# Kernel tuning notes

Hardware: AMD Instinct MI355X
Metric: run time of the kernel (lower is better)

Reference implementation:

```python
import jax, jax.numpy as jnp
import numpy as np

N_EMBD = 1024
N_HEAD = 16
HEAD_DIM = N_EMBD // N_HEAD


def setup_inputs() -> dict:
    key = jax.random.key(0)
    k1, k2, k3, k4, k5 = jax.random.split(key, 5)
    x = jax.random.normal(k1, (4, 2048, N_EMBD), dtype=jnp.float32)
    s = 1.0 / np.sqrt(N_EMBD)
    W_attn = jax.random.normal(k2, (N_EMBD, 3 * N_EMBD), dtype=jnp.float32) * s
    b_attn = jnp.zeros((3 * N_EMBD,), dtype=jnp.float32)
    W_proj = jax.random.normal(k3, (N_EMBD, N_EMBD), dtype=jnp.float32) * s
    b_proj = jnp.zeros((N_EMBD,), dtype=jnp.float32)
    return {"x": x, "W_attn": W_attn, "b_attn": b_attn, "W_proj": W_proj, "b_proj": b_proj}


def _attention(x, W_attn, b_attn, W_proj, b_proj):
    B, T, C = x.shape
    qkv = jnp.einsum("btc,cd->btd", x, W_attn) + b_attn  # [B,T,3C]
    q, k, v = jnp.split(qkv, 3, axis=-1)
    # [B,T,C] -> [B,H,T,D]
    def heads(t):
        return t.reshape(B, T, N_HEAD, HEAD_DIM).transpose(0, 2, 1, 3)
    q, k, v = heads(q), heads(k), heads(v)
    scale = 1.0 / np.sqrt(HEAD_DIM)
    scores = jnp.einsum("bhqd,bhkd->bhqk", q, k) * scale  # [B,H,T,T]
    causal = jnp.tril(jnp.ones((T, T), dtype=bool))
    scores = jnp.where(causal, scores, jnp.finfo(scores.dtype).min)
    attn = jax.nn.softmax(scores, axis=-1)
    y = jnp.einsum("bhqk,bhkd->bhqd", attn, v)  # [B,H,T,D]
    y = y.transpose(0, 2, 1, 3).reshape(B, T, C)
    return jnp.einsum("btc,cd->btd", y, W_proj) + b_proj


def reference(x, W_attn, b_attn, W_proj, b_proj):
    return _attention(x, W_attn, b_attn, W_proj, b_proj)
```

## Files before the change

### kernel.cpp

```cpp
#include <hip/hip_runtime.h>
#include <hip/hip_bf16.h>

#define BB 4
#define TT 2048
#define CC 1024
#define HH 16
#define DD 64
#define BT (BB*TT)
#define C3 (3*CC)
#define LDST 72
#define QSCALE 0.18033688011112042f

typedef __attribute__((ext_vector_type(8))) short short8;
typedef __attribute__((ext_vector_type(4))) float f32x4;

__device__ __forceinline__ short f2bs(float f) {
  __hip_bfloat16 h = __float2bfloat16(f);
  return *reinterpret_cast<short*>(&h);
}

__device__ __forceinline__ void gl_lds16(const short* g, short* l) {
  __builtin_amdgcn_global_load_lds(
      (const __attribute__((address_space(1))) void*)(g),
      (__attribute__((address_space(3))) void*)(l), 16, 0, 0);
}

__global__ __launch_bounds__(256)
void prep(const float* __restrict__ Wa, short* __restrict__ Wat,
          const float* __restrict__ Wp, short* __restrict__ Wpt,
          const float* __restrict__ x, short* __restrict__ Xb)
{
  __shared__ float Lt[64][65];
  const int bx = blockIdx.x;
  if (bx >= 64) {
    size_t chunk = (size_t)(bx - 64) * 16 + blockIdx.y;
    size_t i = (chunk * 256 + threadIdx.x) * 8;
    float4 a = *reinterpret_cast<const float4*>(x + i);
    float4 b = *reinterpret_cast<const float4*>(x + i + 4);
    short8 o;
    o[0] = f2bs(a.x); o[1] = f2bs(a.y); o[2] = f2bs(a.z); o[3] = f2bs(a.w);
    o[4] = f2bs(b.x); o[5] = f2bs(b.y); o[6] = f2bs(b.z); o[7] = f2bs(b.w);
    *reinterpret_cast<short8*>(Xb + i) = o;
    return;
  }
  const bool isA = (bx < 48);
  const float* in  = isA ? Wa  : Wp;
  short*       out = isA ? Wat : Wpt;
  const int N  = isA ? C3 : CC;
  const int n0 = (isA ? bx : bx - 48) * 64;
  const int k0 = blockIdx.y * 64;
  const int cx = threadIdx.x & 15, rr = threadIdx.x >> 4;
#pragma unroll
  for (int p = 0; p < 4; ++p) {
    int kr = p * 16 + rr;
    float4 u = *reinterpret_cast<const float4*>(in + (size_t)(k0 + kr) * N + n0 + cx * 4);
    Lt[kr][cx * 4 + 0] = u.x;
    Lt[kr][cx * 4 + 1] = u.y;
    Lt[kr][cx * 4 + 2] = u.z;
    Lt[kr][cx * 4 + 3] = u.w;
  }
  __syncthreads();
#pragma unroll
  for (int p = 0; p < 4; ++p) {
    int nr = p * 16 + rr;
    short4 o;
    o.x = f2bs(Lt[cx * 4 + 0][nr]);
    o.y = f2bs(Lt[cx * 4 + 1][nr]);
    o.z = f2bs(Lt[cx * 4 + 2][nr]);
    o.w = f2bs(Lt[cx * 4 + 3][nr]);
    *reinterpret_cast<short4*>(out + (size_t)(n0 + nr) * CC + k0 + cx * 4) = o;
  }
}

template<bool QKV>
__global__ __launch_bounds__(512, 2)
void gemm256(const short* __restrict__ A, const short* __restrict__ Bt,
             const float* __restrict__ bias,
             short* __restrict__ qb, short* __restrict__ kb, short* __restrict__ vb,
             float* __restrict__ out)
{
  __shared__ __align__(16) short SMEM[65536];

  const int t = threadIdx.x;
  const int lane = t & 63;
  const int l16 = lane & 15, quad = lane >> 4;
  const int w = t >> 6;
  const int wr = w >> 2, wc = w & 3;

  const int per   = gridDim.x >> 3;
  const int chunk = (blockIdx.x & 7) * per + (blockIdx.x >> 3);
  const int NBC   = QKV ? 12 : 4;
  const int brow  = chunk / NBC, bcol = chunk % NBC;
  const int row0  = brow * 256;
  const int col0  = bcol * 256;

  auto stageQ = [&](int bufS, int kcS, int tileS, bool isA) __attribute__((always_inline)) {
#pragma unroll
    for (int l = 0; l < 2; ++l) {
      int gq = l * 512 + t;
      int rq = gq >> 2;
      int g  = (gq & 3) ^ ((rq >> 1) & 3);
      if (isA) {
        gl_lds16(A + (size_t)(row0 + rq) * CC + tileS * 64 + kcS * 32 + g * 8,
                 &SMEM[bufS * 16384 + kcS * 8192 + gq * 8]);
      } else {
        gl_lds16(Bt + (size_t)(col0 + rq) * CC + tileS * 64 + kcS * 32 + g * 8,
                 &SMEM[32768 + bufS * 16384 + kcS * 8192 + gq * 8]);
      }
    }
  };

  f32x4 acc[8][4];
#pragma unroll
  for (int i = 0; i < 8; ++i)
#pragma unroll
    for (int j = 0; j < 4; ++j) acc[i][j] = (f32x4){0.f, 0.f, 0.f, 0.f};

  auto kTile = [&](int u, int cb, int tm) __attribute__((always_inline)) {
    const short* Ac = &SMEM[cb * 16384];
    const short* Bc = &SMEM[32768 + cb * 16384];
    short8 bf[4];
#pragma unroll
    for (int ph = 0; ph < 4; ++ph) {
      const int kc = ph >> 1, q = ph & 1;
      if (q == 0) {
#pragma unroll
        for (int j = 0; j < 4; ++j) {
          int rb = wc * 64 + j * 16 + l16;
          bf[j] = *reinterpret_cast<const short8*>(
              &Bc[kc * 8192 + rb * 32 + (((quad ^ (rb >> 1)) & 3) << 3)]);
        }
      }
      short8 af[4];
#pragma unroll
      for (int iq = 0; iq < 4; ++iq) {
        int ra = wr * 128 + (q * 4 + iq) * 16 + l16;
        af[iq] = *reinterpret_cast<const short8*>(
            &Ac[kc * 8192 + ra * 32 + (((quad ^ (ra >> 1)) & 3) << 3)]);
      }

      if      (ph == 0) { if (tm < 2) stageQ(cb ^ 1, 1, u + 1, true ); }
      else if (ph == 1) { if (tm < 2) stageQ(cb ^ 1, 1, u + 1, false); }
      else if (ph == 2) { if (tm < 1) stageQ(cb,     0, u + 2, true ); }
      else              { if (tm < 1) stageQ(cb,     0, u + 2, false); }

      __builtin_amdgcn_s_barrier();
      asm volatile("s_waitcnt lgkmcnt(0)" ::: "memory");
      __builtin_amdgcn_sched_barrier(0);

      __builtin_amdgcn_s_setprio(1);
#pragma unroll
      for (int iq = 0; iq < 4; ++iq)
#pragma unroll
        for (int j = 0; j < 4; ++j)
          acc[q * 4 + iq][j] =
              __builtin_amdgcn_mfma_f32_16x16x32_bf16(af[iq], bf[j], acc[q * 4 + iq][j], 0, 0, 0);
      __builtin_amdgcn_s_setprio(0);

      if (ph == 1) {
        if (tm == 2) { asm volatile("s_waitcnt vmcnt(0)" ::: "memory"); }
        else         { asm volatile("s_waitcnt vmcnt(8)" ::: "memory"); }
      } else if (ph == 3) {
        if      (tm == 0) { asm volatile("s_waitcnt vmcnt(8)" ::: "memory"); }
        else if (tm == 1) { asm volatile("s_waitcnt vmcnt(4)" ::: "memory"); }
      }
      __builtin_amdgcn_s_barrier();
    }
  };

  stageQ(0, 0, 0, true);  stageQ(0, 0, 0, false);
  stageQ(0, 1, 0, true);  stageQ(0, 1, 0, false);
  stageQ(1, 0, 1, true);  stageQ(1, 0, 1, false);
  asm volatile("s_waitcnt vmcnt(8)" ::: "memory");
  __builtin_amdgcn_s_barrier();

  for (int u = 0; u < 14; u += 2) {
    kTile(u,     0, 0);
    kTile(u + 1, 1, 0);
  }
  kTile(14, 0, 1);
  kTile(15, 1, 2);

  if constexpr (QKV) {
    const int sel = col0 >> 10;
#pragma unroll
    for (int hp = 0; hp < 2; ++hp) {
      __syncthreads();
      if (wr == hp) {
#pragma unroll
        for (int j = 0; j < 4; ++j) {
          const int colL = wc * 64 + j * 16 + l16;
          const float bv = bias[col0 + colL];
#pragma unroll
          for (int i = 0; i < 8; ++i)
#pragma unroll
            for (int r = 0; r < 4; ++r) {
              const int rl = i * 16 + quad * 4 + r;
              float val = acc[i][j][r] + bv;
              if (sel == 0) val *= QSCALE;
              short vs = f2bs(val);
              if (sel == 2) {
                int tpl = (rl & ~63) | ((rl & 15) << 2) | ((rl >> 4) & 3);
                SMEM[colL * 136 + tpl] = vs;
              } else {
                SMEM[rl * 264 + colL] = vs;
              }
            }
        }
      }
      __syncthreads();
      const int Rbase = row0 + hp * 128;
      const int bi = Rbase >> 11;
      if (sel != 2) {
        short* __restrict__ dstB = (sel == 0) ? qb : kb;
#pragma unroll
        for (int rep = 0; rep < 8; ++rep) {
          int slot = rep * 512 + t;
          int rl = slot >> 5, ch = slot & 31;
          short8 vv = *reinterpret_cast<const short8*>(&SMEM[rl * 264 + ch * 8]);
          int tt  = (Rbase & 2047) + rl;
          int cin = (col0 + ch * 8) & 1023;
          int h = cin >> 6, dd = cin & 63;
          *reinterpret_cast<short8*>(
              &dstB[(((size_t)(bi * HH + h)) * TT + tt) * DD + dd]) = vv;
        }
      } else {
#pragma unroll
        for (int rep = 0; rep < 8; ++rep) {
          int slot = rep * 512 + t;
          int dcol = slot >> 4, ch = slot & 15;
          short8 vv = *reinterpret_cast<const short8*>(&SMEM[dcol * 136 + ch * 8]);
          int cin = (col0 + dcol) & 1023;
          int h = cin >> 6, dd = cin & 63;
          int ttb = (Rbase & 2047) + ch * 8;
          *reinterpret_cast<short8*>(
              &vb[(((size_t)(bi * HH + h)) * DD + dd) * TT + ttb]) = vv;
        }
      }
    }
  } else {
#pragma unroll
    for (int j = 0; j < 4; ++j) {
      int col = col0 + wc * 64 + j * 16 + l16;
      float bv = bias[col];
#pragma unroll
      for (int i = 0; i < 8; ++i)
#pragma unroll
        for (int r = 0; r < 4; ++r) {
          int row = row0 + wr * 128 + i * 16 + quad * 4 + r;
          out[(size_t)row * CC + col] = acc[i][j][r] + bv;
        }
    }
  }
}

__global__ __launch_bounds__(256, 4)
void attn_mfma(const short* __restrict__ Qb, const short* __restrict__ Kb,
               const short* __restrict__ Vb, short* __restrict__ Y)
{
  __shared__ __align__(16) short Ks[64 * LDST];
  __shared__ __align__(16) short Vt[64 * LDST];
  __shared__ __align__(16) short Pw[4 * 16 * LDST];

  const int t    = threadIdx.x;
  const int w    = t >> 6;
  const int lane = t & 63;
  const int l16  = lane & 15;
  const int quad = lane >> 4;

  const int linear = blockIdx.x + 16 * (blockIdx.y + 16 * blockIdx.z);
  const int nb  = (linear & 7) * 128 + (linear >> 3);
  const int qt0 = nb & 15;
  const int h   = (nb >> 4) & 15;
  const int bi  = nb >> 8;
  const size_t head = (size_t)(bi * HH + h) * TT * DD;

  short* myP = &Pw[w * 16 * LDST];
  const int sr = t >> 2;
  const int sc = (t & 3) << 4;

  const int qts[2] = { qt0, 31 - qt0 };

#pragma unroll
  for (int half = 0; half < 2; ++half) {
    const int qt = qts[half];
    const int q0 = qt * 64;

    short8 qf[2];
#pragma unroll
    for (int kc = 0; kc < 2; ++kc)
      qf[kc] = *reinterpret_cast<const short8*>(
          &Qb[head + (size_t)(q0 + w * 16 + l16) * DD + kc * 32 + quad * 8]);

    f32x4 O[4];
#pragma unroll
    for (int dt = 0; dt < 4; ++dt) O[dt] = (f32x4){0.f, 0.f, 0.f, 0.f};
    float lsum[4] = {};

    for (int kt = 0; kt <= qt; ++kt) {
      const int k0 = kt * 64;
      __syncthreads();

      {
        const short* kg = Kb + head + (size_t)(k0 + sr) * DD + sc;
        short8 a = *reinterpret_cast<const short8*>(kg);
        short8 b = *reinterpret_cast<const short8*>(kg + 8);
        *reinterpret_cast<short8*>(&Ks[sr * LDST + sc])     = a;
        *reinterpret_cast<short8*>(&Ks[sr * LDST + sc + 8]) = b;
        const short* vg = Vb + head + (size_t)sr * TT + k0 + sc;
        short8 c = *reinterpret_cast<const short8*>(vg);
        short8 d = *reinterpret_cast<const short8*>(vg + 8);
        *reinterpret_cast<short8*>(&Vt[sr * LDST + sc])     = c;
        *reinterpret_cast<short8*>(&Vt[sr * LDST + sc + 8]) = d;
      }
      __syncthreads();

      short8 kf[4][2];
#pragma unroll
      for (int nt = 0; nt < 4; ++nt)
#pragma unroll
        for (int kc = 0; kc < 2; ++kc)
          kf[nt][kc] = *reinterpret_cast<const short8*>(
              &Ks[(nt * 16 + l16) * LDST + kc * 32 + quad * 8]);

      f32x4 s[4];
#pragma unroll
      for (int nt = 0; nt < 4; ++nt) s[nt] = (f32x4){0.f, 0.f, 0.f, 0.f};
      __builtin_amdgcn_s_setprio(1);
#pragma unroll
      for (int nt = 0; nt < 4; ++nt)
#pragma unroll
        for (int kc = 0; kc < 2; ++kc)
          s[nt] = __builtin_amdgcn_mfma_f32_16x16x32_bf16(qf[kc], kf[nt][kc], s[nt], 0, 0, 0);
      __builtin_amdgcn_s_setprio(0);

      const int rowg_base = q0 + w * 16 + quad * 4;
#pragma unroll
      for (int r = 0; r < 4; ++r) {
        const int rowg = rowg_base + r;
        short pk[4];
#pragma unroll
        for (int nt = 0; nt < 4; ++nt) {
          float e = (k0 + nt * 16 + l16 <= rowg) ? __builtin_amdgcn_exp2f(s[nt][r]) : 0.f;
          lsum[r] += e;
          pk[nt] = f2bs(e);
        }
        short4 p4; p4.x = pk[0]; p4.y = pk[1]; p4.z = pk[2]; p4.w = pk[3];
        *reinterpret_cast<short4*>(&myP[(quad * 4 + r) * LDST + (l16 << 2)]) = p4;
      }

      __builtin_amdgcn_s_setprio(1);
#pragma unroll
      for (int cc = 0; cc < 2; ++cc) {
        short8 pf = *reinterpret_cast<const short8*>(
            &myP[l16 * LDST + cc * 32 + quad * 8]);
#pragma unroll
        for (int dt = 0; dt < 4; ++dt) {
          short8 vf = *reinterpret_cast<const short8*>(
              &Vt[(dt * 16 + l16) * LDST + cc * 32 + quad * 8]);
          O[dt] = __builtin_amdgcn_mfma_f32_16x16x32_bf16(pf, vf, O[dt], 0, 0, 0);
        }
      }
      __builtin_amdgcn_s_setprio(0);
    }

    float linv[4];
#pragma unroll
    for (int r = 0; r < 4; ++r) {
      float s = lsum[r];
      s += __shfl_xor(s, 1);
      s += __shfl_xor(s, 2);
      s += __shfl_xor(s, 4);
      s += __shfl_xor(s, 8);
      linv[r] = 1.f / s;
    }
#pragma unroll
    for (int dt = 0; dt < 4; ++dt)
#pragma unroll
      for (int r = 0; r < 4; ++r) {
        int tg = q0 + w * 16 + quad * 4 + r;
        Y[((size_t)bi * TT + tg) * CC + h * DD + dt * 16 + l16] =
            f2bs(O[dt][r] * linv[r]);
      }
  }
}

extern "C" void kernel_launch(void* const* d_in, const int* in_sizes, int n_in,
                              void* d_out, int out_size, void* d_ws, size_t ws_size,
                              hipStream_t stream) {
  const float* x  = (const float*)d_in[0];
  const float* Wa = (const float*)d_in[1];
  const float* ba = (const float*)d_in[2];
  const float* Wp = (const float*)d_in[3];
  const float* bp = (const float*)d_in[4];
  float* out = (float*)d_out;

  const size_t NELT = (size_t)BB * HH * TT * DD;
  short* qb  = (short*)d_ws;
  short* kb  = qb + NELT;
  short* vb  = kb + NELT;
  short* Xb  = vb + NELT;
  short* Wat = Xb  + (size_t)BT * CC;
  short* Wpt = Wat + (size_t)CC * C3;
  short* Yb  = Wpt + (size_t)CC * CC;

  prep<<<dim3(64 + 256, 16), 256, 0, stream>>>(Wa, Wat, Wp, Wpt, x, Xb);

  gemm256<true> <<<dim3((C3 / 256) * (BT / 256)), 512, 0, stream>>>(Xb, Wat, ba, qb, kb, vb, nullptr);
  attn_mfma     <<<dim3(16, HH, BB),              256, 0, stream>>>(qb, kb, vb, Yb);
  gemm256<false><<<dim3((CC / 256) * (BT / 256)), 512, 0, stream>>>(Yb, Wpt, bp, nullptr, nullptr, nullptr, out);
}
```

Measured before the change: 270.2 us.

## Pre-swizzle K/V tiles for async LDS loads in attention; narrow projection GEMM tiles

```diff
diff --git a/kernel.cpp b/kernel.cpp
--- a/kernel.cpp
+++ b/kernel.cpp
@@ -72,14 +72,16 @@
   }
 }
 
-template<bool QKV>
+template<bool QKV, int NBF>
 __global__ __launch_bounds__(512, 2)
 void gemm256(const short* __restrict__ A, const short* __restrict__ Bt,
              const float* __restrict__ bias,
              short* __restrict__ qb, short* __restrict__ kb, short* __restrict__ vb,
              float* __restrict__ out)
 {
-  __shared__ __align__(16) short SMEM[65536];
+  constexpr int BQ   = NBF * 64 * 32;
+  constexpr int BOFF = 32768;
+  __shared__ __align__(16) short SMEM[BOFF + 4 * BQ];
 
   const int t = threadIdx.x;
   const int lane = t & 63;
@@ -89,46 +91,51 @@
 
   const int per   = gridDim.x >> 3;
   const int chunk = (blockIdx.x & 7) * per + (blockIdx.x >> 3);
-  const int NBC   = QKV ? 12 : 4;
+  const int NBC   = QKV ? 12 : (CC / (NBF * 64));
   const int brow  = chunk / NBC, bcol = chunk % NBC;
   const int row0  = brow * 256;
-  const int col0  = bcol * 256;
-
-  auto stageQ = [&](int bufS, int kcS, int tileS, bool isA) __attribute__((always_inline)) {
+  const int col0  = bcol * (NBF * 64);
+
+  auto stageQA = [&](int bufS, int kcS, int tileS) __attribute__((always_inline)) {
 #pragma unroll
     for (int l = 0; l < 2; ++l) {
       int gq = l * 512 + t;
       int rq = gq >> 2;
       int g  = (gq & 3) ^ ((rq >> 1) & 3);
-      if (isA) {
-        gl_lds16(A + (size_t)(row0 + rq) * CC + tileS * 64 + kcS * 32 + g * 8,
-                 &SMEM[bufS * 16384 + kcS * 8192 + gq * 8]);
-      } else {
-        gl_lds16(Bt + (size_t)(col0 + rq) * CC + tileS * 64 + kcS * 32 + g * 8,
-                 &SMEM[32768 + bufS * 16384 + kcS * 8192 + gq * 8]);
-      }
+      gl_lds16(A + (size_t)(row0 + rq) * CC + tileS * 64 + kcS * 32 + g * 8,
+               &SMEM[bufS * 16384 + kcS * 8192 + gq * 8]);
     }
   };
-
-  f32x4 acc[8][4];
+  auto stageQB = [&](int bufS, int kcS, int tileS) __attribute__((always_inline)) {
+#pragma unroll
+    for (int l = 0; l < NBF / 2; ++l) {
+      int gq = l * 512 + t;
+      int rq = gq >> 2;
+      int g  = (gq & 3) ^ ((rq >> 1) & 3);
+      gl_lds16(Bt + (size_t)(col0 + rq) * CC + tileS * 64 + kcS * 32 + g * 8,
+               &SMEM[BOFF + bufS * 2 * BQ + kcS * BQ + gq * 8]);
+    }
+  };
+
+  f32x4 acc[8][NBF];
 #pragma unroll
   for (int i = 0; i < 8; ++i)
 #pragma unroll
-    for (int j = 0; j < 4; ++j) acc[i][j] = (f32x4){0.f, 0.f, 0.f, 0.f};
+    for (int j = 0; j < NBF; ++j) acc[i][j] = (f32x4){0.f, 0.f, 0.f, 0.f};
 
   auto kTile = [&](int u, int cb, int tm) __attribute__((always_inline)) {
     const short* Ac = &SMEM[cb * 16384];
-    const short* Bc = &SMEM[32768 + cb * 16384];
-    short8 bf[4];
+    const short* Bc = &SMEM[BOFF + cb * 2 * BQ];
+    short8 bf[NBF];
 #pragma unroll
     for (int ph = 0; ph < 4; ++ph) {
       const int kc = ph >> 1, q = ph & 1;
       if (q == 0) {
 #pragma unroll
-        for (int j = 0; j < 4; ++j) {
-          int rb = wc * 64 + j * 16 + l16;
+        for (int j = 0; j < NBF; ++j) {
+          int rb = wc * (NBF * 16) + j * 16 + l16;
           bf[j] = *reinterpret_cast<const short8*>(
-              &Bc[kc * 8192 + rb * 32 + (((quad ^ (rb >> 1)) & 3) << 3)]);
+              &Bc[kc * BQ + rb * 32 + (((quad ^ (rb >> 1)) & 3) << 3)]);
         }
       }
       short8 af[4];
@@ -139,10 +146,10 @@
             &Ac[kc * 8192 + ra * 32 + (((quad ^ (ra >> 1)) & 3) << 3)]);
       }
 
-      if      (ph == 0) { if (tm < 2) stageQ(cb ^ 1, 1, u + 1, true ); }
-      else if (ph == 1) { if (tm < 2) stageQ(cb ^ 1, 1, u + 1, false); }
-      else if (ph == 2) { if (tm < 1) stageQ(cb,     0, u + 2, true ); }
-      else              { if (tm < 1) stageQ(cb,     0, u + 2, false); }
+      if      (ph == 0) { if (tm < 2) stageQA(cb ^ 1, 1, u + 1); }
+      else if (ph == 1) { if (tm < 2) stageQB(cb ^ 1, 1, u + 1); }
+      else if (ph == 2) { if (tm < 1) stageQA(cb,     0, u + 2); }
+      else              { if (tm < 1) stageQB(cb,     0, u + 2); }
 
       __builtin_amdgcn_s_barrier();
       asm volatile("s_waitcnt lgkmcnt(0)" ::: "memory");
@@ -152,26 +159,33 @@
 #pragma unroll
       for (int iq = 0; iq < 4; ++iq)
 #pragma unroll
-        for (int j = 0; j < 4; ++j)
+        for (int j = 0; j < NBF; ++j)
           acc[q * 4 + iq][j] =
               __builtin_amdgcn_mfma_f32_16x16x32_bf16(af[iq], bf[j], acc[q * 4 + iq][j], 0, 0, 0);
       __builtin_amdgcn_s_setprio(0);
 
       if (ph == 1) {
         if (tm == 2) { asm volatile("s_waitcnt vmcnt(0)" ::: "memory"); }
-        else         { asm volatile("s_waitcnt vmcnt(8)" ::: "memory"); }
+        else if (NBF == 4) { asm volatile("s_waitcnt vmcnt(8)" ::: "memory"); }
+        else               { asm volatile("s_waitcnt vmcnt(6)" ::: "memory"); }
       } else if (ph == 3) {
-        if      (tm == 0) { asm volatile("s_waitcnt vmcnt(8)" ::: "memory"); }
-        else if (tm == 1) { asm volatile("s_waitcnt vmcnt(4)" ::: "memory"); }
+        if (tm == 0) {
+          if (NBF == 4) { asm volatile("s_waitcnt vmcnt(8)" ::: "memory"); }
+          else          { asm volatile("s_waitcnt vmcnt(6)" ::: "memory"); }
+        } else if (tm == 1) {
+          if (NBF == 4) { asm volatile("s_waitcnt vmcnt(4)" ::: "memory"); }
+          else          { asm volatile("s_waitcnt vmcnt(3)" ::: "memory"); }
+        }
       }
       __builtin_amdgcn_s_barrier();
     }
   };
 
-  stageQ(0, 0, 0, true);  stageQ(0, 0, 0, false);
-  stageQ(0, 1, 0, true);  stageQ(0, 1, 0, false);
-  stageQ(1, 0, 1, true);  stageQ(1, 0, 1, false);
-  asm volatile("s_waitcnt vmcnt(8)" ::: "memory");
+  stageQA(0, 0, 0);  stageQB(0, 0, 0);
+  stageQA(0, 1, 0);  stageQB(0, 1, 0);
+  stageQA(1, 0, 1);  stageQB(1, 0, 1);
+  if (NBF == 4) { asm volatile("s_waitcnt vmcnt(8)" ::: "memory"); }
+  else          { asm volatile("s_waitcnt vmcnt(6)" ::: "memory"); }
   __builtin_amdgcn_s_barrier();
 
   for (int u = 0; u < 14; u += 2) {
@@ -211,8 +225,7 @@
       __syncthreads();
       const int Rbase = row0 + hp * 128;
       const int bi = Rbase >> 11;
-      if (sel != 2) {
-        short* __restrict__ dstB = (sel == 0) ? qb : kb;
+      if (sel == 0) {
 #pragma unroll
         for (int rep = 0; rep < 8; ++rep) {
           int slot = rep * 512 + t;
@@ -220,9 +233,23 @@
           short8 vv = *reinterpret_cast<const short8*>(&SMEM[rl * 264 + ch * 8]);
           int tt  = (Rbase & 2047) + rl;
           int cin = (col0 + ch * 8) & 1023;
-          int h = cin >> 6, dd = cin & 63;
+          int hh = cin >> 6, dd = cin & 63;
           *reinterpret_cast<short8*>(
-              &dstB[(((size_t)(bi * HH + h)) * TT + tt) * DD + dd]) = vv;
+              &qb[(((size_t)(bi * HH + hh)) * TT + tt) * DD + dd]) = vv;
+        }
+      } else if (sel == 1) {
+#pragma unroll
+        for (int rep = 0; rep < 8; ++rep) {
+          int slot = rep * 512 + t;
+          int rl = slot >> 5, ch = slot & 31;
+          short8 vv = *reinterpret_cast<const short8*>(&SMEM[rl * 264 + ch * 8]);
+          int tt  = (Rbase & 2047) + rl;
+          int cin = (col0 + ch * 8) & 1023;
+          int hh = cin >> 6;
+          int rt = tt & 63;
+          int cs = ((cin >> 3) & 7) ^ ((rt >> 1) & 7);
+          size_t tile = (size_t)(bi * HH + hh) * 32 + (tt >> 6);
+          *reinterpret_cast<short8*>(&kb[tile * 4096 + rt * 64 + cs * 8]) = vv;
         }
       } else {
 #pragma unroll
@@ -231,17 +258,18 @@
           int dcol = slot >> 4, ch = slot & 15;
           short8 vv = *reinterpret_cast<const short8*>(&SMEM[dcol * 136 + ch * 8]);
           int cin = (col0 + dcol) & 1023;
-          int h = cin >> 6, dd = cin & 63;
-          int ttb = (Rbase & 2047) + ch * 8;
+          int hh = cin >> 6, dd = cin & 63;
+          int ktv = ((Rbase & 2047) >> 6) + (ch >> 3);
+          int cs  = (ch & 7) ^ ((dd >> 1) & 7);
           *reinterpret_cast<short8*>(
-              &vb[(((size_t)(bi * HH + h)) * DD + dd) * TT + ttb]) = vv;
+              &vb[((size_t)(bi * HH + hh) * 32 + ktv) * 4096 + dd * 64 + cs * 8]) = vv;
         }
       }
     }
   } else {
 #pragma unroll
-    for (int j = 0; j < 4; ++j) {
-      int col = col0 + wc * 64 + j * 16 + l16;
+    for (int j = 0; j < NBF; ++j) {
+      int col = col0 + wc * (NBF * 16) + j * 16 + l16;
       float bv = bias[col];
 #pragma unroll
       for (int i = 0; i < 8; ++i)
@@ -258,8 +286,8 @@
 void attn_mfma(const short* __restrict__ Qb, const short* __restrict__ Kb,
                const short* __restrict__ Vb, short* __restrict__ Y)
 {
-  __shared__ __align__(16) short Ks[64 * LDST];
-  __shared__ __align__(16) short Vt[64 * LDST];
+  __shared__ __align__(16) short Kd[2][4096];
+  __shared__ __align__(16) short Vt[4096];
   __shared__ __align__(16) short Pw[4 * 16 * LDST];
 
   const int t    = threadIdx.x;
@@ -276,8 +304,17 @@
   const size_t head = (size_t)(bi * HH + h) * TT * DD;
 
   short* myP = &Pw[w * 16 * LDST];
-  const int sr = t >> 2;
-  const int sc = (t & 3) << 4;
+
+  auto stageK = [&](int kt, int p) __attribute__((always_inline)) {
+    const short* src = Kb + head + (size_t)kt * 4096;
+    gl_lds16(src + t * 8,        &Kd[p][t * 8]);
+    gl_lds16(src + 2048 + t * 8, &Kd[p][2048 + t * 8]);
+  };
+  auto stageV = [&](int kt) __attribute__((always_inline)) {
+    const short* src = Vb + head + (size_t)kt * 4096;
+    gl_lds16(src + t * 8,        &Vt[t * 8]);
+    gl_lds16(src + 2048 + t * 8, &Vt[2048 + t * 8]);
+  };
 
   const int qts[2] = { qt0, 31 - qt0 };
 
@@ -297,31 +334,30 @@
     for (int dt = 0; dt < 4; ++dt) O[dt] = (f32x4){0.f, 0.f, 0.f, 0.f};
     float lsum[4] = {};
 
+    stageK(0, 0);
+    stageV(0);
+    if (qt >= 1) {
+      stageK(1, 1);
+      asm volatile("s_waitcnt vmcnt(4)" ::: "memory");
+    } else {
+      asm volatile("s_waitcnt vmcnt(2)" ::: "memory");
+    }
+    __builtin_amdgcn_s_barrier();
+
     for (int kt = 0; kt <= qt; ++kt) {
+      const int p  = kt & 1;
       const int k0 = kt * 64;
-      __syncthreads();
-
-      {
-        const short* kg = Kb + head + (size_t)(k0 + sr) * DD + sc;
-        short8 a = *reinterpret_cast<const short8*>(kg);
-        short8 b = *reinterpret_cast<const short8*>(kg + 8);
-        *reinterpret_cast<short8*>(&Ks[sr * LDST + sc])     = a;
-        *reinterpret_cast<short8*>(&Ks[sr * LDST + sc + 8]) = b;
-        const short* vg = Vb + head + (size_t)sr * TT + k0 + sc;
-        short8 c = *reinterpret_cast<const short8*>(vg);
-        short8 d = *reinterpret_cast<const short8*>(vg + 8);
-        *reinterpret_cast<short8*>(&Vt[sr * LDST + sc])     = c;
-        *reinterpret_cast<short8*>(&Vt[sr * LDST + sc + 8]) = d;
-      }
-      __syncthreads();
 
       short8 kf[4][2];
 #pragma unroll
       for (int nt = 0; nt < 4; ++nt)
 #pragma unroll
-        for (int kc = 0; kc < 2; ++kc)
+        for (int kc = 0; kc < 2; ++kc) {
+          int r = nt * 16 + l16;
+          int c = kc * 4 + quad;
           kf[nt][kc] = *reinterpret_cast<const short8*>(
-              &Ks[(nt * 16 + l16) * LDST + kc * 32 + quad * 8]);
+              &Kd[p][r * 64 + ((c ^ ((r >> 1) & 7)) << 3)]);
+        }
 
       f32x4 s[4];
 #pragma unroll
@@ -349,6 +385,11 @@
         *reinterpret_cast<short4*>(&myP[(quad * 4 + r) * LDST + (l16 << 2)]) = p4;
       }
 
+      asm volatile("s_waitcnt vmcnt(0)" ::: "memory");
+      __builtin_amdgcn_s_barrier();
+
+      if (kt + 2 <= qt) stageK(kt + 2, p);
+
       __builtin_amdgcn_s_setprio(1);
 #pragma unroll
       for (int cc = 0; cc < 2; ++cc) {
@@ -356,12 +397,17 @@
             &myP[l16 * LDST + cc * 32 + quad * 8]);
 #pragma unroll
         for (int dt = 0; dt < 4; ++dt) {
+          int r = dt * 16 + l16;
+          int c = cc * 4 + quad;
           short8 vf = *reinterpret_cast<const short8*>(
-              &Vt[(dt * 16 + l16) * LDST + cc * 32 + quad * 8]);
+              &Vt[r * 64 + ((c ^ ((r >> 1) & 7)) << 3)]);
           O[dt] = __builtin_amdgcn_mfma_f32_16x16x32_bf16(pf, vf, O[dt], 0, 0, 0);
         }
       }
       __builtin_amdgcn_s_setprio(0);
+
+      __builtin_amdgcn_s_barrier();
+      if (kt + 1 <= qt) stageV(kt + 1);
     }
 
     float linv[4];
@@ -406,7 +452,7 @@
 
   prep<<<dim3(64 + 256, 16), 256, 0, stream>>>(Wa, Wat, Wp, Wpt, x, Xb);
 
-  gemm256<true> <<<dim3((C3 / 256) * (BT / 256)), 512, 0, stream>>>(Xb, Wat, ba, qb, kb, vb, nullptr);
-  attn_mfma     <<<dim3(16, HH, BB),              256, 0, stream>>>(qb, kb, vb, Yb);
-  gemm256<false><<<dim3((CC / 256) * (BT / 256)), 512, 0, stream>>>(Yb, Wpt, bp, nullptr, nullptr, nullptr, out);
-}
+  gemm256<true, 4> <<<dim3((C3 / 256) * (BT / 256)), 512, 0, stream>>>(Xb, Wat, ba, qb, kb, vb, nullptr);
+  attn_mfma        <<<dim3(16, HH, BB),              256, 0, stream>>>(qb, kb, vb, Yb);
+  gemm256<false, 2><<<dim3((CC / 128) * (BT / 256)), 512, 0, stream>>>(Yb, Wpt, bp, nullptr, nullptr, nullptr, out);
+}
```

New measurement: 250.9 us. 1.08x faster.
